# Performance work log

Hardware: AMD Instinct MI355X
Metric: run time of the kernel (lower is better)

The kernel has to match this reference:

```python
import jax, jax.numpy as jnp
import numpy as np


def _conv1x1(x, w, b):
    # x: [B, Cin, H, W]; w: [Cout, Cin, 1, 1]; b: [Cout]
    y = jnp.einsum('bchw,oc->bohw', x, w[:, :, 0, 0])
    return y + b[None, :, None, None]


def setup_inputs() -> dict:
    key = jax.random.key(0)
    ks = jax.random.split(key, 9)
    B, C, H, W = 8, 256, 64, 64
    Cq = C // 4
    sc = 0.05
    return {
        'x': jax.random.normal(ks[0], (B, C, H, W), jnp.float32),
        'query_weight': jax.random.normal(ks[1], (Cq, C, 1, 1), jnp.float32) * sc,
        'query_bias': jax.random.normal(ks[2], (Cq,), jnp.float32) * sc,
        'key_weight': jax.random.normal(ks[3], (Cq, C, 1, 1), jnp.float32) * sc,
        'key_bias': jax.random.normal(ks[4], (Cq,), jnp.float32) * sc,
        'value_weight': jax.random.normal(ks[5], (C, C, 1, 1), jnp.float32) * sc,
        'value_bias': jax.random.normal(ks[6], (C,), jnp.float32) * sc,
        'gamma_weight': jax.random.normal(ks[7], (C, C, 1, 1), jnp.float32) * sc,
        'gamma_bias': jax.random.normal(ks[8], (C,), jnp.float32) * sc,
    }


def reference(x, query_weight, query_bias, key_weight, key_bias,
              value_weight, value_bias, gamma_weight, gamma_bias):
    B, C, H, W = x.shape
    N = H * W
    q = _conv1x1(x, query_weight, query_bias).reshape(B, -1, N)   # [B, Cq, N]
    k = _conv1x1(x, key_weight, key_bias).reshape(B, -1, N)       # [B, Cq, N]
    v = _conv1x1(x, value_weight, value_bias).reshape(B, C, N)    # [B, C, N]
    # energy[b, i, j] = sum_c q[b, c, i] * k[b, c, j]
    energy = jnp.einsum('bci,bcj->bij', q, k)                     # [B, N, N]
    energy = jax.nn.elu(energy) / N
    out = jnp.einsum('bcn,bnm->bcm', v, energy).reshape(B, C, H, W)
    return _conv1x1(out, gamma_weight, gamma_bias)
```

## Files before the change

### kernel.cpp

```cpp
#include <hip/hip_runtime.h>
#include <cmath>

#define BB 8
#define CC 256
#define CQ 64
#define NN 4096
constexpr float INV_N = 1.0f / 4096.0f;

typedef __attribute__((ext_vector_type(8))) short short8;
typedef __attribute__((ext_vector_type(4))) short short4v;
typedef __attribute__((ext_vector_type(4))) float float4v;

__device__ __forceinline__ short f2bf(float f) {
  union { float f; unsigned u; } x; x.f = f;
  unsigned r = x.u + 0x7fffu + ((x.u >> 16) & 1u);
  return (short)(r >> 16);
}

__global__ __launch_bounds__(256) void prep_kernel(
    const float* __restrict__ wq, const float* __restrict__ wk,
    const float* __restrict__ wv, const float* __restrict__ wg,
    const float* __restrict__ bv,
    short* __restrict__ wqbf, short* __restrict__ wkbf,
    short* __restrict__ wvpbf, float* __restrict__ bvp) {
  const int bx = blockIdx.x;
  const int tid = threadIdx.x;
  if (bx < 64) {
    const int o0 = (bx >> 3) * 32, c0 = (bx & 7) * 32;
    const int cc = tid & 31, oo = tid >> 5;
    float acc[4] = {0.f, 0.f, 0.f, 0.f};
    for (int u = 0; u < 256; ++u) {
      const float xv = wv[(size_t)u * 256 + c0 + cc];
#pragma unroll
      for (int i = 0; i < 4; ++i)
        acc[i] += wg[(size_t)(o0 + oo * 4 + i) * 256 + u] * xv;
    }
#pragma unroll
    for (int i = 0; i < 4; ++i)
      wvpbf[(size_t)(o0 + oo * 4 + i) * 256 + c0 + cc] = f2bf(acc[i]);
  } else if (bx == 64) {
#pragma unroll 4
    for (int t = 0; t < 16; ++t) {
      const int idx = (t * 256 + tid) * 4;
      const float4 a = *reinterpret_cast<const float4*>(&wq[idx]);
      short4v p; p.x = f2bf(a.x); p.y = f2bf(a.y); p.z = f2bf(a.z); p.w = f2bf(a.w);
      *reinterpret_cast<short4v*>(&wqbf[idx]) = p;
      const float4 b4 = *reinterpret_cast<const float4*>(&wk[idx]);
      short4v q4; q4.x = f2bf(b4.x); q4.y = f2bf(b4.y); q4.z = f2bf(b4.z); q4.w = f2bf(b4.w);
      *reinterpret_cast<short4v*>(&wkbf[idx]) = q4;
    }
  } else {
    float acc = 0.f;
    for (int u = 0; u < 256; ++u) acc += wg[(size_t)tid * 256 + u] * bv[u];
    bvp[tid] = acc;
  }
}

__global__ __launch_bounds__(256, 4) void qkv_kernel(
    const float* __restrict__ X,
    const short* __restrict__ wqbf, const short* __restrict__ wkbf,
    const short* __restrict__ wvpbf,
    const float* __restrict__ bq, const float* __restrict__ bk,
    const float* __restrict__ bvp,
    short* __restrict__ qt, short* __restrict__ kt, short* __restrict__ vt) {
  __shared__ short smem[8448 + 2560];
  short* xt = smem;
  short* Os = smem + 8448;

  const int tid = threadIdx.x;
  const int wid = tid >> 6;
  const int lane = tid & 63, quad = lane >> 4, l16 = lane & 15;
  const int b = blockIdx.x, n0 = blockIdx.y * 32;

#pragma unroll
  for (int p = 0; p < 2; ++p) {
    const int idx = p * 256 + tid;
    const int cg = idx >> 3;
    const int ng = idx & 7;
    float4 xr[4];
#pragma unroll
    for (int j = 0; j < 4; ++j)
      xr[j] = *reinterpret_cast<const float4*>(
          &X[((size_t)b * CC + cg * 4 + j) * NN + n0 + ng * 4]);
    const int colbase = (((cg >> 1) ^ ng) * 8 + (cg & 1) * 4);
#pragma unroll
    for (int r = 0; r < 4; ++r) {
      short4v pk;
      pk.x = f2bf((&xr[0].x)[r]); pk.y = f2bf((&xr[1].x)[r]);
      pk.z = f2bf((&xr[2].x)[r]); pk.w = f2bf((&xr[3].x)[r]);
      *reinterpret_cast<short4v*>(&xt[(ng * 4 + r) * 264 + colbase]) = pk;
    }
  }
  __syncthreads();

  const short* Wsrc[6] = {wqbf, wkbf, wvpbf, wvpbf + 64 * 256,
                          wvpbf + 128 * 256, wvpbf + 192 * 256};
  const int arow = wid * 16 + l16;

#pragma unroll
  for (int ch = 0; ch < 6; ++ch) {
    float4v acc2[2];
    acc2[0] = float4v{0.f, 0.f, 0.f, 0.f};
    acc2[1] = float4v{0.f, 0.f, 0.f, 0.f};
#pragma unroll
    for (int kk = 0; kk < 8; ++kk) {
      const short8 a = *reinterpret_cast<const short8*>(
          &Wsrc[ch][(size_t)arow * 256 + kk * 32 + quad * 8]);
#pragma unroll
      for (int tm = 0; tm < 2; ++tm) {
        const int row = tm * 16 + l16;
        const int swr = (row >> 2) & 7;
        const short8 bfrag = *reinterpret_cast<const short8*>(
            &xt[row * 264 + ((kk * 4 + quad) ^ swr) * 8]);
        acc2[tm] = __builtin_amdgcn_mfma_f32_16x16x32_bf16(a, bfrag,
                                                           acc2[tm], 0, 0, 0);
      }
    }

    if (ch < 2) {
      const float* bias = (ch == 0) ? bq : bk;
      const float4v bv4 = *reinterpret_cast<const float4v*>(
          &bias[wid * 16 + quad * 4]);
      short* dst = (ch == 0) ? qt : kt;
#pragma unroll
      for (int tm = 0; tm < 2; ++tm) {
        short4v pk;
#pragma unroll
        for (int r = 0; r < 4; ++r) pk[r] = f2bf(acc2[tm][r] + bv4[r]);
        *reinterpret_cast<short4v*>(
            &dst[((size_t)b * NN + n0 + tm * 16 + l16) * 64 + wid * 16 +
                 quad * 4]) = pk;
      }
    } else {
      const float4v bv4 = *reinterpret_cast<const float4v*>(
          &bvp[(ch - 2) * 64 + wid * 16 + quad * 4]);
      __syncthreads();
#pragma unroll
      for (int tm = 0; tm < 2; ++tm)
#pragma unroll
        for (int r = 0; r < 4; ++r)
          Os[(wid * 16 + quad * 4 + r) * 40 + tm * 16 + l16] =
              f2bf(acc2[tm][r] + bv4[r]);
      __syncthreads();
      const int o = tid >> 2, ng = (tid & 3) * 8;
      const short8 s0 = *reinterpret_cast<const short8*>(&Os[o * 40 + ng]);
      *reinterpret_cast<short8*>(
          &vt[((size_t)b * CC + (ch - 2) * 64 + o) * NN + n0 + ng]) = s0;
    }
  }
}

__global__ __launch_bounds__(256, 4) void attn_kernel(
    const short* __restrict__ qt, const short* __restrict__ kt,
    const short* __restrict__ vt, const float* __restrict__ bg,
    float* __restrict__ out) {
  __shared__ short Es[2][64 * 72];

  const int tid = threadIdx.x;
  const int wid = tid >> 6;
  const int lane = tid & 63, quad = lane >> 4, l16 = lane & 15;
  const int chalf = blockIdx.x;
  const int m0 = blockIdx.y * 64;
  const int b = blockIdx.z;

  short8 kf[4][2];
#pragma unroll
  for (int tm = 0; tm < 4; ++tm)
#pragma unroll
    for (int kk = 0; kk < 2; ++kk)
      kf[tm][kk] = *reinterpret_cast<const short8*>(
          &kt[((size_t)b * NN + m0 + tm * 16 + l16) * 64 + kk * 32 + quad * 8]);

  const short* qrow = &qt[((size_t)b * NN + wid * 16 + l16) * 64 + quad * 8];
  const short* vrow[2];
#pragma unroll
  for (int tc = 0; tc < 2; ++tc)
    vrow[tc] = &vt[((size_t)b * CC + chalf * 128 + wid * 32 + tc * 16 + l16) *
                       NN + quad * 8];

  float4v acc[2][4];
#pragma unroll
  for (int i = 0; i < 2; ++i)
#pragma unroll
    for (int j = 0; j < 4; ++j) acc[i][j] = float4v{0.f, 0.f, 0.f, 0.f};

  short8 aq0 = *reinterpret_cast<const short8*>(qrow);
  short8 aq1 = *reinterpret_cast<const short8*>(qrow + 32);
  {
    float4v s[4];
#pragma unroll
    for (int tm = 0; tm < 4; ++tm) {
      float4v t = {0.f, 0.f, 0.f, 0.f};
      t = __builtin_amdgcn_mfma_f32_16x16x32_bf16(aq0, kf[tm][0], t, 0, 0, 0);
      t = __builtin_amdgcn_mfma_f32_16x16x32_bf16(aq1, kf[tm][1], t, 0, 0, 0);
      s[tm] = t;
    }
#pragma unroll
    for (int tm = 0; tm < 4; ++tm) {
      short4v pk;
#pragma unroll
      for (int r = 0; r < 4; ++r) {
        float sv = s[tm][r];
        sv = (sv > 0.f) ? sv : (__expf(sv) - 1.f);
        pk[r] = f2bf(sv * INV_N);
      }
      *reinterpret_cast<short4v*>(
          &Es[0][(tm * 16 + l16) * 72 + wid * 16 + quad * 4]) = pk;
    }
  }
  short8 av[2][2];
#pragma unroll
  for (int tc = 0; tc < 2; ++tc) {
    av[tc][0] = *reinterpret_cast<const short8*>(vrow[tc]);
    av[tc][1] = *reinterpret_cast<const short8*>(vrow[tc] + 32);
  }
  aq0 = *reinterpret_cast<const short8*>(qrow + 64 * 64);
  aq1 = *reinterpret_cast<const short8*>(qrow + 64 * 64 + 32);
  __syncthreads();

  for (int it = 0; it < 64; ++it) {
    const int rb = it & 1, wb = rb ^ 1;

    float4v s[4];
#pragma unroll
    for (int tm = 0; tm < 4; ++tm) {
      float4v t = {0.f, 0.f, 0.f, 0.f};
      t = __builtin_amdgcn_mfma_f32_16x16x32_bf16(aq0, kf[tm][0], t, 0, 0, 0);
      t = __builtin_amdgcn_mfma_f32_16x16x32_bf16(aq1, kf[tm][1], t, 0, 0, 0);
      s[tm] = t;
    }
#pragma unroll
    for (int tm = 0; tm < 4; ++tm) {
      short4v pk;
#pragma unroll
      for (int r = 0; r < 4; ++r) {
        float sv = s[tm][r];
        sv = (sv > 0.f) ? sv : (__expf(sv) - 1.f);
        pk[r] = f2bf(sv * INV_N);
      }
      *reinterpret_cast<short4v*>(
          &Es[wb][(tm * 16 + l16) * 72 + wid * 16 + quad * 4]) = pk;
    }

#pragma unroll
    for (int tm = 0; tm < 4; ++tm) {
      const short8 be0 = *reinterpret_cast<const short8*>(
          &Es[rb][(tm * 16 + l16) * 72 + quad * 8]);
      const short8 be1 = *reinterpret_cast<const short8*>(
          &Es[rb][(tm * 16 + l16) * 72 + 32 + quad * 8]);
#pragma unroll
      for (int tc = 0; tc < 2; ++tc) {
        acc[tc][tm] = __builtin_amdgcn_mfma_f32_16x16x32_bf16(
            av[tc][0], be0, acc[tc][tm], 0, 0, 0);
        acc[tc][tm] = __builtin_amdgcn_mfma_f32_16x16x32_bf16(
            av[tc][1], be1, acc[tc][tm], 0, 0, 0);
      }
    }

    {
      const size_t nb = (size_t)(it + 1) * 64;
#pragma unroll
      for (int tc = 0; tc < 2; ++tc) {
        av[tc][0] = *reinterpret_cast<const short8*>(vrow[tc] + nb);
        av[tc][1] = *reinterpret_cast<const short8*>(vrow[tc] + nb + 32);
      }
      aq0 = *reinterpret_cast<const short8*>(qrow + (size_t)(it + 2) * 64 * 64);
      aq1 = *reinterpret_cast<const short8*>(qrow + (size_t)(it + 2) * 64 * 64 + 32);
    }
    __syncthreads();
  }

#pragma unroll
  for (int tc = 0; tc < 2; ++tc) {
#pragma unroll
    for (int r = 0; r < 4; ++r) {
      const int c = chalf * 128 + wid * 32 + tc * 16 + quad * 4 + r;
      const float bgv = bg[c];
#pragma unroll
      for (int tm = 0; tm < 4; ++tm) {
        out[((size_t)b * CC + c) * NN + m0 + tm * 16 + l16] =
            acc[tc][tm][r] + bgv;
      }
    }
  }
}

extern "C" void kernel_launch(void* const* d_in, const int* in_sizes, int n_in,
                              void* d_out, int out_size, void* d_ws,
                              size_t ws_size, hipStream_t stream) {
  const float* x  = (const float*)d_in[0];
  const float* wq = (const float*)d_in[1];
  const float* bq = (const float*)d_in[2];
  const float* wk = (const float*)d_in[3];
  const float* bk = (const float*)d_in[4];
  const float* wv = (const float*)d_in[5];
  const float* bv = (const float*)d_in[6];
  const float* wg = (const float*)d_in[7];
  const float* bg = (const float*)d_in[8];
  float* out = (float*)d_out;

  short* qt    = (short*)d_ws;
  short* kt    = qt + (size_t)BB * NN * CQ;
  short* vt    = kt + (size_t)BB * NN * CQ;
  short* wqbf  = vt + (size_t)BB * CC * NN;
  short* wkbf  = wqbf + (size_t)CQ * CC;
  short* wvpbf = wkbf + (size_t)CQ * CC;
  float* bvp   = (float*)(wvpbf + (size_t)CC * CC);

  prep_kernel<<<dim3(66), 256, 0, stream>>>(wq, wk, wv, wg, bv,
                                            wqbf, wkbf, wvpbf, bvp);
  qkv_kernel<<<dim3(BB, NN / 32), 256, 0, stream>>>(
      x, wqbf, wkbf, wvpbf, bq, bk, bvp, qt, kt, vt);
  attn_kernel<<<dim3(2, NN / 64, BB), 256, 0, stream>>>(qt, kt, vt, bg, out);
}
```

Measured before the change: 315.7 us.

## Fuse channel halves in attention, each wave owns all channels; prefetch QKV weights

The attention kernel no longer splits output channels across two blocks. Each block handles all 256 channels for 64 columns, and each wave owns a 16-column slice, so the energy tile is computed once instead of twice. V fragments are now read straight from global memory inside the loop, 16 channel tiles per wave, rather than prefetched, and the kernel is pinned to 2 waves per EU to fit the 16 accumulators. The QKV kernel software-pipelines its weight fragment loads across output chunks, at the cost of more register pressure and possibly exposed global-load latency in the attention loop.

Result: slower. 612.5 us (+94.0%).

```diff
diff --git a/kernel.cpp b/kernel.cpp
--- a/kernel.cpp
+++ b/kernel.cpp
@@ -56,7 +56,8 @@
   }
 }
 
-__global__ __launch_bounds__(256, 4) void qkv_kernel(
+__global__ __launch_bounds__(256)
+__attribute__((amdgpu_waves_per_eu(4, 4))) void qkv_kernel(
     const float* __restrict__ X,
     const short* __restrict__ wqbf, const short* __restrict__ wkbf,
     const short* __restrict__ wvpbf,
@@ -72,6 +73,16 @@
   const int lane = tid & 63, quad = lane >> 4, l16 = lane & 15;
   const int b = blockIdx.x, n0 = blockIdx.y * 32;
 
+  const short* Wsrc[6] = {wqbf, wkbf, wvpbf, wvpbf + 64 * 256,
+                          wvpbf + 128 * 256, wvpbf + 192 * 256};
+  const int arow = wid * 16 + l16;
+
+  short8 curA[4];
+#pragma unroll
+  for (int kk = 0; kk < 4; ++kk)
+    curA[kk] = *reinterpret_cast<const short8*>(
+        &Wsrc[0][(size_t)arow * 256 + kk * 32 + quad * 8]);
+
 #pragma unroll
   for (int p = 0; p < 2; ++p) {
     const int idx = p * 256 + tid;
@@ -93,26 +104,45 @@
   }
   __syncthreads();
 
-  const short* Wsrc[6] = {wqbf, wkbf, wvpbf, wvpbf + 64 * 256,
-                          wvpbf + 128 * 256, wvpbf + 192 * 256};
-  const int arow = wid * 16 + l16;
-
 #pragma unroll
   for (int ch = 0; ch < 6; ++ch) {
+    short8 hiA[4];
+#pragma unroll
+    for (int kk = 0; kk < 4; ++kk)
+      hiA[kk] = *reinterpret_cast<const short8*>(
+          &Wsrc[ch][(size_t)arow * 256 + (kk + 4) * 32 + quad * 8]);
+
     float4v acc2[2];
     acc2[0] = float4v{0.f, 0.f, 0.f, 0.f};
     acc2[1] = float4v{0.f, 0.f, 0.f, 0.f};
-#pragma unroll
-    for (int kk = 0; kk < 8; ++kk) {
-      const short8 a = *reinterpret_cast<const short8*>(
-          &Wsrc[ch][(size_t)arow * 256 + kk * 32 + quad * 8]);
+
+#pragma unroll
+    for (int kk = 0; kk < 4; ++kk) {
 #pragma unroll
       for (int tm = 0; tm < 2; ++tm) {
         const int row = tm * 16 + l16;
         const int swr = (row >> 2) & 7;
         const short8 bfrag = *reinterpret_cast<const short8*>(
             &xt[row * 264 + ((kk * 4 + quad) ^ swr) * 8]);
-        acc2[tm] = __builtin_amdgcn_mfma_f32_16x16x32_bf16(a, bfrag,
+        acc2[tm] = __builtin_amdgcn_mfma_f32_16x16x32_bf16(curA[kk], bfrag,
+                                                           acc2[tm], 0, 0, 0);
+      }
+    }
+    if (ch < 5) {
+#pragma unroll
+      for (int kk = 0; kk < 4; ++kk)
+        curA[kk] = *reinterpret_cast<const short8*>(
+            &Wsrc[ch + 1][(size_t)arow * 256 + kk * 32 + quad * 8]);
+    }
+#pragma unroll
+    for (int kk = 4; kk < 8; ++kk) {
+#pragma unroll
+      for (int tm = 0; tm < 2; ++tm) {
+        const int row = tm * 16 + l16;
+        const int swr = (row >> 2) & 7;
+        const short8 bfrag = *reinterpret_cast<const short8*>(
+            &xt[row * 264 + ((kk * 4 + quad) ^ swr) * 8]);
+        acc2[tm] = __builtin_amdgcn_mfma_f32_16x16x32_bf16(hiA[kk - 4], bfrag,
                                                            acc2[tm], 0, 0, 0);
       }
     }
@@ -150,7 +180,8 @@
   }
 }
 
-__global__ __launch_bounds__(256, 4) void attn_kernel(
+__global__ __launch_bounds__(256)
+__attribute__((amdgpu_waves_per_eu(2, 2))) void attn_kernel(
     const short* __restrict__ qt, const short* __restrict__ kt,
     const short* __restrict__ vt, const float* __restrict__ bg,
     float* __restrict__ out) {
@@ -159,9 +190,8 @@
   const int tid = threadIdx.x;
   const int wid = tid >> 6;
   const int lane = tid & 63, quad = lane >> 4, l16 = lane & 15;
-  const int chalf = blockIdx.x;
-  const int m0 = blockIdx.y * 64;
-  const int b = blockIdx.z;
+  const int m0 = blockIdx.x * 64;
+  const int b = blockIdx.y;
 
   short8 kf[4][2];
 #pragma unroll
@@ -172,17 +202,11 @@
           &kt[((size_t)b * NN + m0 + tm * 16 + l16) * 64 + kk * 32 + quad * 8]);
 
   const short* qrow = &qt[((size_t)b * NN + wid * 16 + l16) * 64 + quad * 8];
-  const short* vrow[2];
-#pragma unroll
-  for (int tc = 0; tc < 2; ++tc)
-    vrow[tc] = &vt[((size_t)b * CC + chalf * 128 + wid * 32 + tc * 16 + l16) *
-                       NN + quad * 8];
-
-  float4v acc[2][4];
-#pragma unroll
-  for (int i = 0; i < 2; ++i)
-#pragma unroll
-    for (int j = 0; j < 4; ++j) acc[i][j] = float4v{0.f, 0.f, 0.f, 0.f};
+  const short* vbase = &vt[((size_t)b * CC + l16) * NN + quad * 8];
+
+  float4v acc[16];
+#pragma unroll
+  for (int i = 0; i < 16; ++i) acc[i] = float4v{0.f, 0.f, 0.f, 0.f};
 
   short8 aq0 = *reinterpret_cast<const short8*>(qrow);
   short8 aq1 = *reinterpret_cast<const short8*>(qrow + 32);
@@ -208,12 +232,6 @@
           &Es[0][(tm * 16 + l16) * 72 + wid * 16 + quad * 4]) = pk;
     }
   }
-  short8 av[2][2];
-#pragma unroll
-  for (int tc = 0; tc < 2; ++tc) {
-    av[tc][0] = *reinterpret_cast<const short8*>(vrow[tc]);
-    av[tc][1] = *reinterpret_cast<const short8*>(vrow[tc] + 32);
-  }
   aq0 = *reinterpret_cast<const short8*>(qrow + 64 * 64);
   aq1 = *reinterpret_cast<const short8*>(qrow + 64 * 64 + 32);
   __syncthreads();
@@ -242,45 +260,35 @@
           &Es[wb][(tm * 16 + l16) * 72 + wid * 16 + quad * 4]) = pk;
     }
 
-#pragma unroll
-    for (int tm = 0; tm < 4; ++tm) {
-      const short8 be0 = *reinterpret_cast<const short8*>(
-          &Es[rb][(tm * 16 + l16) * 72 + quad * 8]);
-      const short8 be1 = *reinterpret_cast<const short8*>(
-          &Es[rb][(tm * 16 + l16) * 72 + 32 + quad * 8]);
-#pragma unroll
-      for (int tc = 0; tc < 2; ++tc) {
-        acc[tc][tm] = __builtin_amdgcn_mfma_f32_16x16x32_bf16(
-            av[tc][0], be0, acc[tc][tm], 0, 0, 0);
-        acc[tc][tm] = __builtin_amdgcn_mfma_f32_16x16x32_bf16(
-            av[tc][1], be1, acc[tc][tm], 0, 0, 0);
-      }
-    }
-
-    {
-      const size_t nb = (size_t)(it + 1) * 64;
-#pragma unroll
-      for (int tc = 0; tc < 2; ++tc) {
-        av[tc][0] = *reinterpret_cast<const short8*>(vrow[tc] + nb);
-        av[tc][1] = *reinterpret_cast<const short8*>(vrow[tc] + nb + 32);
-      }
-      aq0 = *reinterpret_cast<const short8*>(qrow + (size_t)(it + 2) * 64 * 64);
-      aq1 = *reinterpret_cast<const short8*>(qrow + (size_t)(it + 2) * 64 * 64 + 32);
-    }
+    const short8 be0 = *reinterpret_cast<const short8*>(
+        &Es[rb][(wid * 16 + l16) * 72 + quad * 8]);
+    const short8 be1 = *reinterpret_cast<const short8*>(
+        &Es[rb][(wid * 16 + l16) * 72 + 32 + quad * 8]);
+    const short* vn = vbase + (size_t)it * 64;
+#pragma unroll
+    for (int tc = 0; tc < 16; ++tc) {
+      const short8 av0 =
+          *reinterpret_cast<const short8*>(vn + (size_t)tc * 16 * NN);
+      const short8 av1 =
+          *reinterpret_cast<const short8*>(vn + (size_t)tc * 16 * NN + 32);
+      acc[tc] = __builtin_amdgcn_mfma_f32_16x16x32_bf16(av0, be0, acc[tc], 0, 0, 0);
+      acc[tc] = __builtin_amdgcn_mfma_f32_16x16x32_bf16(av1, be1, acc[tc], 0, 0, 0);
+    }
+
+    aq0 = *reinterpret_cast<const short8*>(qrow + (size_t)(it + 2) * 64 * 64);
+    aq1 = *reinterpret_cast<const short8*>(qrow + (size_t)(it + 2) * 64 * 64 + 32);
     __syncthreads();
   }
 
 #pragma unroll
-  for (int tc = 0; tc < 2; ++tc) {
+  for (int tc = 0; tc < 16; ++tc) {
+    const float4v bg4 =
+        *reinterpret_cast<const float4v*>(&bg[tc * 16 + quad * 4]);
 #pragma unroll
     for (int r = 0; r < 4; ++r) {
-      const int c = chalf * 128 + wid * 32 + tc * 16 + quad * 4 + r;
-      const float bgv = bg[c];
-#pragma unroll
-      for (int tm = 0; tm < 4; ++tm) {
-        out[((size_t)b * CC + c) * NN + m0 + tm * 16 + l16] =
-            acc[tc][tm][r] + bgv;
-      }
+      const int c = tc * 16 + quad * 4 + r;
+      out[((size_t)b * CC + c) * NN + m0 + wid * 16 + l16] =
+          acc[tc][r] + bg4[r];
     }
   }
 }
@@ -311,5 +319,5 @@
                                             wqbf, wkbf, wvpbf, bvp);
   qkv_kernel<<<dim3(BB, NN / 32), 256, 0, stream>>>(
       x, wqbf, wkbf, wvpbf, bq, bk, bvp, qt, kt, vt);
-  attn_kernel<<<dim3(2, NN / 64, BB), 256, 0, stream>>>(qt, kt, vt, bg, out);
-}
+  attn_kernel<<<dim3(NN / 64, BB), 256, 0, stream>>>(qt, kt, vt, bg, out);
+}
```
